# Performance work log

Hardware: AMD Instinct MI355X
Metric: run time of the kernel (lower is better)

The kernel has to match this reference:

```python
import jax, jax.numpy as jnp
import numpy as np

LAMBDA = 0.01  # LM damping (lambda_ init arg)
KEPS = 1000.0 * 2.220446049250313e-16  # same constant as torch likelihood_v2


def setup_inputs() -> dict:
    key = jax.random.key(0)
    k1, k2, k3, k4 = jax.random.split(key, 4)
    B, K, H, W, P = 8192, 6, 16, 16, 5
    # strictly positive expected photon counts
    mu = jax.random.uniform(k1, (B, K, H, W), jnp.float32, 0.5, 100.0)
    # noisy, non-negative samples around mu (Poisson-like)
    smp = jnp.maximum(mu + 5.0 * jax.random.normal(k2, (B, K, H, W), jnp.float32), 0.0)
    dmudtheta = jax.random.normal(k3, (B, K, H, W, P), jnp.float32)
    cur = jax.random.normal(k4, (B, P), jnp.float32)
    prmm = jnp.stack([jnp.full((P,), -1e5, jnp.float32),
                      jnp.full((P,), 1e5, jnp.float32)], axis=1)  # [P,2]
    return {"smp": smp, "mu": mu, "dmudtheta": dmudtheta,
            "cur": cur, "param_range_min_max": prmm}


def reference(smp, mu, dmudtheta, cur, param_range_min_max):
    # likelihood_v2 (simflux=True: reduce over last 3 sample dims), varfit=0
    mupos = jnp.where(mu > 0, mu, jnp.where(mu < 0, KEPS, 0.0))
    weight = (smp - mupos) / mupos                  # [B,K,H,W]
    dweight = smp / (mupos * mupos)                 # [B,K,H,W]
    logL = jnp.sum(smp * jnp.log(mupos) - mupos, axis=(-3, -2, -1))   # [B]
    gradlogL = jnp.einsum('bkhw,bkhwp->bp', weight, dmudtheta)        # [B,P]
    # fused 5x5 Hessian: one pass over the jacobian instead of 25 sums
    HessianlogL = -jnp.einsum('bkhw,bkhwp,bkhwq->bpq', dweight,
                              dmudtheta, dmudtheta)                   # [B,P,P]
    # MLE_instead_lmupdate: LM-damped Newton step
    diag = jnp.diagonal(HessianlogL, axis1=-2, axis2=-1)              # [B,P]
    P = diag.shape[-1]
    Bmat = HessianlogL + LAMBDA * diag[..., None] * jnp.eye(P, dtype=diag.dtype)
    dtheta = jnp.linalg.solve(-Bmat, gradlogL[..., None])[..., 0]     # [B,P]
    dtheta = jnp.where(jnp.isnan(dtheta), -0.1 * cur, dtheta)
    new_cur = cur + dtheta
    new_cur = jnp.maximum(new_cur, param_range_min_max[None, :, 0])
    new_cur = jnp.minimum(new_cur, param_range_min_max[None, :, 1])
    # pack updated params and logL so all reductions stay live: [B, P+1]
    return jnp.concatenate([new_cur, logL[:, None]], axis=-1)
```

## Files before the change

### kernel.cpp

```cpp
#include <hip/hip_runtime.h>
#include <math.h>

#define KEPS 2.220446049250313e-13f
#define LAMBDA 0.01f

#define NPIX 1536
#define NP 5

__global__ __launch_bounds__(256) void lm_mle_simflux_kernel(
    const float* __restrict__ smp,
    const float* __restrict__ mu,
    const float* __restrict__ dmu,
    const float* __restrict__ cur,
    const float* __restrict__ prmm,
    float* __restrict__ out,
    int B)
{
    const int lane = threadIdx.x & 63;
    const int wv   = threadIdx.x >> 6;
    const int b    = (blockIdx.x << 2) + wv;
    if (b >= B) return;

    const float* sb = smp + (size_t)b * NPIX;
    const float* mb = mu  + (size_t)b * NPIX;
    const float* jb = dmu + (size_t)b * NPIX * NP;

    float g0 = 0.f, g1 = 0.f, g2 = 0.f, g3 = 0.f, g4 = 0.f;
    float S[15];
    #pragma unroll
    for (int i = 0; i < 15; ++i) S[i] = 0.f;
    float logL = 0.f;

    for (int it = 0; it < 6; ++it) {
        const int pix0 = ((it << 6) + lane) << 2;
        const float4 s4 = *reinterpret_cast<const float4*>(sb + pix0);
        const float4 m4 = *reinterpret_cast<const float4*>(mb + pix0);
        const float* jp = jb + (size_t)pix0 * NP;
        const float4 ja = *reinterpret_cast<const float4*>(jp + 0);
        const float4 jv1 = *reinterpret_cast<const float4*>(jp + 4);
        const float4 jc = *reinterpret_cast<const float4*>(jp + 8);
        const float4 jd = *reinterpret_cast<const float4*>(jp + 12);
        const float4 je = *reinterpret_cast<const float4*>(jp + 16);

        const float v[20] = {ja.x, ja.y, ja.z, ja.w,
                             jv1.x, jv1.y, jv1.z, jv1.w,
                             jc.x, jc.y, jc.z, jc.w,
                             jd.x, jd.y, jd.z, jd.w,
                             je.x, je.y, je.z, je.w};
        const float sm[4] = {s4.x, s4.y, s4.z, s4.w};
        const float mm[4] = {m4.x, m4.y, m4.z, m4.w};

        #pragma unroll
        for (int k = 0; k < 4; ++k) {
            const float m  = mm[k];
            const float mp = (m > 0.f) ? m : ((m < 0.f) ? KEPS : 0.f);
            const float s  = sm[k];
            const float r  = __builtin_amdgcn_rcpf(mp);
            const float w  = (s - mp) * r;
            const float dw = s * r * r;
            logL = fmaf(s, __logf(mp), logL) - mp;

            const float j0 = v[5*k+0], j1 = v[5*k+1], j2 = v[5*k+2],
                        j3 = v[5*k+3], j4 = v[5*k+4];
            g0 = fmaf(w, j0, g0);
            g1 = fmaf(w, j1, g1);
            g2 = fmaf(w, j2, g2);
            g3 = fmaf(w, j3, g3);
            g4 = fmaf(w, j4, g4);
            const float t0 = dw * j0, t1 = dw * j1, t2 = dw * j2,
                        t3 = dw * j3, t4 = dw * j4;
            S[0]  = fmaf(t0, j0, S[0]);
            S[1]  = fmaf(t1, j0, S[1]);
            S[2]  = fmaf(t1, j1, S[2]);
            S[3]  = fmaf(t2, j0, S[3]);
            S[4]  = fmaf(t2, j1, S[4]);
            S[5]  = fmaf(t2, j2, S[5]);
            S[6]  = fmaf(t3, j0, S[6]);
            S[7]  = fmaf(t3, j1, S[7]);
            S[8]  = fmaf(t3, j2, S[8]);
            S[9]  = fmaf(t3, j3, S[9]);
            S[10] = fmaf(t4, j0, S[10]);
            S[11] = fmaf(t4, j1, S[11]);
            S[12] = fmaf(t4, j2, S[12]);
            S[13] = fmaf(t4, j3, S[13]);
            S[14] = fmaf(t4, j4, S[14]);
        }
    }

    #pragma unroll
    for (int off = 32; off > 0; off >>= 1) {
        logL += __shfl_xor(logL, off, 64);
        g0 += __shfl_xor(g0, off, 64);
        g1 += __shfl_xor(g1, off, 64);
        g2 += __shfl_xor(g2, off, 64);
        g3 += __shfl_xor(g3, off, 64);
        g4 += __shfl_xor(g4, off, 64);
        #pragma unroll
        for (int i = 0; i < 15; ++i) S[i] += __shfl_xor(S[i], off, 64);
    }

    float A[5][5];
    A[0][0] = S[0] * (1.f + LAMBDA);
    A[1][0] = S[1];  A[0][1] = S[1];
    A[1][1] = S[2] * (1.f + LAMBDA);
    A[2][0] = S[3];  A[0][2] = S[3];
    A[2][1] = S[4];  A[1][2] = S[4];
    A[2][2] = S[5] * (1.f + LAMBDA);
    A[3][0] = S[6];  A[0][3] = S[6];
    A[3][1] = S[7];  A[1][3] = S[7];
    A[3][2] = S[8];  A[2][3] = S[8];
    A[3][3] = S[9] * (1.f + LAMBDA);
    A[4][0] = S[10]; A[0][4] = S[10];
    A[4][1] = S[11]; A[1][4] = S[11];
    A[4][2] = S[12]; A[2][4] = S[12];
    A[4][3] = S[13]; A[3][4] = S[13];
    A[4][4] = S[14] * (1.f + LAMBDA);

    float x[5] = {g0, g1, g2, g3, g4};

    #pragma unroll
    for (int c = 0; c < 5; ++c) {
        const float inv = 1.0f / A[c][c];
        #pragma unroll
        for (int r2 = c + 1; r2 < 5; ++r2) {
            const float f = A[r2][c] * inv;
            #pragma unroll
            for (int q = c; q < 5; ++q) A[r2][q] = fmaf(-f, A[c][q], A[r2][q]);
            x[r2] = fmaf(-f, x[c], x[r2]);
        }
    }
    #pragma unroll
    for (int r2 = 4; r2 >= 0; --r2) {
        float acc = x[r2];
        #pragma unroll
        for (int q = r2 + 1; q < 5; ++q) acc = fmaf(-A[r2][q], x[q], acc);
        x[r2] = acc / A[r2][r2];
    }

    if (lane == 0) {
        float* ob = out + (size_t)b * 6;
        #pragma unroll
        for (int p = 0; p < 5; ++p) {
            float dt = x[p];
            const float c = cur[(size_t)b * NP + p];
            if (dt != dt) dt = -0.1f * c;
            float nc = c + dt;
            const float lo = prmm[2 * p];
            const float hi = prmm[2 * p + 1];
            nc = fminf(fmaxf(nc, lo), hi);
            ob[p] = nc;
        }
        ob[5] = logL;
    }
}

extern "C" void kernel_launch(void* const* d_in, const int* in_sizes, int n_in,
                              void* d_out, int out_size, void* d_ws, size_t ws_size,
                              hipStream_t stream) {
    const float* smp  = (const float*)d_in[0];
    const float* mu   = (const float*)d_in[1];
    const float* dmu  = (const float*)d_in[2];
    const float* cur  = (const float*)d_in[3];
    const float* prmm = (const float*)d_in[4];
    float* out = (float*)d_out;

    const int B = in_sizes[3] / NP;
    const int blocks = (B + 3) / 4;
    lm_mle_simflux_kernel<<<blocks, 256, 0, stream>>>(smp, mu, dmu, cur, prmm, out, B);
}
```

Measured before the change: 68.17 us.

## Double-buffer global loads with nontemporal hints and split logL accumulation

Software-pipelines the per-wave loop by prefetching the next iteration's sample, mu and jacobian vectors into a second register buffer while the current one is computed, and fully unrolls the loop. The loads now use nontemporal hints because the streamed data is not reused. The logL accumulation is split into a log2-weighted sum and a separate mu sum, combined once with ln2 after the reduction, which removes a multiply from the inner loop. In exchange the kernel uses more registers, which may lower occupancy, and the different summation order changes floating-point rounding slightly.

```diff
diff --git a/kernel.cpp b/kernel.cpp
--- a/kernel.cpp
+++ b/kernel.cpp
@@ -3,9 +3,11 @@
 
 #define KEPS 2.220446049250313e-13f
 #define LAMBDA 0.01f
-
 #define NPIX 1536
 #define NP 5
+#define LN2F 0.69314718055994530942f
+
+typedef float f32x4 __attribute__((ext_vector_type(4)));
 
 __global__ __launch_bounds__(256) void lm_mle_simflux_kernel(
     const float* __restrict__ smp,
@@ -29,24 +31,38 @@
     float S[15];
     #pragma unroll
     for (int i = 0; i < 15; ++i) S[i] = 0.f;
-    float logL = 0.f;
+    float logLa = 0.f;
+    float logLb = 0.f;
 
+    f32x4 sB[2], mB[2], jB[2][5];
+
+    auto LOAD = [&](int buf, int it) {
+        const int pix0 = ((it << 6) + lane) << 2;
+        sB[buf] = __builtin_nontemporal_load(
+            reinterpret_cast<const f32x4*>(sb + pix0));
+        mB[buf] = __builtin_nontemporal_load(
+            reinterpret_cast<const f32x4*>(mb + pix0));
+        const float* jp = jb + (size_t)pix0 * NP;
+        #pragma unroll
+        for (int q = 0; q < 5; ++q)
+            jB[buf][q] = __builtin_nontemporal_load(
+                reinterpret_cast<const f32x4*>(jp + 4 * q));
+    };
+
+    LOAD(0, 0);
+
+    #pragma unroll
     for (int it = 0; it < 6; ++it) {
-        const int pix0 = ((it << 6) + lane) << 2;
-        const float4 s4 = *reinterpret_cast<const float4*>(sb + pix0);
-        const float4 m4 = *reinterpret_cast<const float4*>(mb + pix0);
-        const float* jp = jb + (size_t)pix0 * NP;
-        const float4 ja = *reinterpret_cast<const float4*>(jp + 0);
-        const float4 jv1 = *reinterpret_cast<const float4*>(jp + 4);
-        const float4 jc = *reinterpret_cast<const float4*>(jp + 8);
-        const float4 jd = *reinterpret_cast<const float4*>(jp + 12);
-        const float4 je = *reinterpret_cast<const float4*>(jp + 16);
+        const int cb = it & 1;
+        if (it < 5) LOAD(cb ^ 1, it + 1);
 
-        const float v[20] = {ja.x, ja.y, ja.z, ja.w,
-                             jv1.x, jv1.y, jv1.z, jv1.w,
-                             jc.x, jc.y, jc.z, jc.w,
-                             jd.x, jd.y, jd.z, jd.w,
-                             je.x, je.y, je.z, je.w};
+        const f32x4 s4 = sB[cb];
+        const f32x4 m4 = mB[cb];
+        const float v[20] = {jB[cb][0].x, jB[cb][0].y, jB[cb][0].z, jB[cb][0].w,
+                             jB[cb][1].x, jB[cb][1].y, jB[cb][1].z, jB[cb][1].w,
+                             jB[cb][2].x, jB[cb][2].y, jB[cb][2].z, jB[cb][2].w,
+                             jB[cb][3].x, jB[cb][3].y, jB[cb][3].z, jB[cb][3].w,
+                             jB[cb][4].x, jB[cb][4].y, jB[cb][4].z, jB[cb][4].w};
         const float sm[4] = {s4.x, s4.y, s4.z, s4.w};
         const float mm[4] = {m4.x, m4.y, m4.z, m4.w};
 
@@ -58,7 +74,8 @@
             const float r  = __builtin_amdgcn_rcpf(mp);
             const float w  = (s - mp) * r;
             const float dw = s * r * r;
-            logL = fmaf(s, __logf(mp), logL) - mp;
+            logLa = fmaf(s, __log2f(mp), logLa);
+            logLb += mp;
 
             const float j0 = v[5*k+0], j1 = v[5*k+1], j2 = v[5*k+2],
                         j3 = v[5*k+3], j4 = v[5*k+4];
@@ -89,7 +106,8 @@
 
     #pragma unroll
     for (int off = 32; off > 0; off >>= 1) {
-        logL += __shfl_xor(logL, off, 64);
+        logLa += __shfl_xor(logLa, off, 64);
+        logLb += __shfl_xor(logLb, off, 64);
         g0 += __shfl_xor(g0, off, 64);
         g1 += __shfl_xor(g1, off, 64);
         g2 += __shfl_xor(g2, off, 64);
@@ -98,6 +116,7 @@
         #pragma unroll
         for (int i = 0; i < 15; ++i) S[i] += __shfl_xor(S[i], off, 64);
     }
+    const float logL = fmaf(LN2F, logLa, -logLb);
 
     float A[5][5];
     A[0][0] = S[0] * (1.f + LAMBDA);
```

Measured after the change: 115.1 us. 68.9% more time.
